# Kernel optimization log

Hardware: AMD Instinct MI355X
Metric: run time of the kernel (lower is better)

The kernel has to match this reference:

```python
import jax, jax.numpy as jnp
import numpy as np

B = 65536
HID = 256
C_K, C_V, C_S, NQ = 4, 8, 4, 4
EMB_OUT = 64  # state_embedding_size - 1


def _spatial_basis():
    # h = w = 5, U = V = 2 -> [5,5,4] Fourier basis
    ph = jnp.arange(1.0, 6.0)[:, None] * jnp.ones((1, 5)) * (np.pi / 5.0)
    pw = jnp.ones((5, 1)) * jnp.arange(1.0, 6.0)[None, :] * (np.pi / 5.0)
    u = jnp.arange(1.0, 3.0)[None, :]
    a = jnp.cos(ph[:, :, None] * u)  # [5,5,2]
    b = jnp.cos(pw[:, :, None] * u)  # [5,5,2]
    return jnp.einsum('hwu,hwv->hwuv', a, b).reshape(5, 5, 4).astype(jnp.float32)


def _conv(x, w, b):
    # x: NHWC, w: HWIO, pad=1, stride=1
    y = jax.lax.conv_general_dilated(x, w, window_strides=(1, 1), padding=[(1, 1), (1, 1)],
                                     dimension_numbers=('NHWC', 'HWIO', 'NHWC'))
    return y + b


def setup_inputs() -> dict:
    key = jax.random.key(0)
    ks = jax.random.split(key, 20)
    s = 0.05
    inp = {
        'X': jax.random.normal(ks[0], (B, 7, 7, 3), jnp.float32),
        'upper_module_hidden_state': jax.random.normal(ks[1], (B, HID), jnp.float32),
        'c1_w': jax.random.normal(ks[2], (5, 5, 3, 8), jnp.float32) * s,
        'c1_b': jax.random.normal(ks[3], (8,), jnp.float32) * s,
        'c2_w': jax.random.normal(ks[4], (3, 3, 8, 12), jnp.float32) * s,
        'c2_b': jax.random.normal(ks[5], (12,), jnp.float32) * s,
    }
    qdims = [(HID, 256), (256, 128), (128, 64), (64, 32), (32, 32)]
    for i, (din, dout) in enumerate(qdims):
        inp[f'qw{i}'] = jax.random.normal(ks[6 + 2 * i], (din, dout), jnp.float32) * s
        inp[f'qb{i}'] = jax.random.normal(ks[7 + 2 * i], (dout,), jnp.float32) * s
    inp['aw0'] = jax.random.normal(ks[16], ((C_V + C_S) * NQ, 32), jnp.float32) * s
    inp['ab0'] = jax.random.normal(ks[17], (32,), jnp.float32) * s
    inp['aw1'] = jax.random.normal(ks[18], (32, EMB_OUT), jnp.float32) * s
    inp['ab1'] = jax.random.normal(ks[19], (EMB_OUT,), jnp.float32) * s
    return inp


def reference(X, upper_module_hidden_state, c1_w, c1_b, c2_w, c2_b,
              qw0, qb0, qw1, qb1, qw2, qb2, qw3, qb3, qw4, qb4,
              aw0, ab0, aw1, ab1):
    b = X.shape[0]
    # vision CNN: [b,7,7,3] -> [b,5,5,8] -> [b,5,5,12]
    O = _conv(_conv(X, c1_w, c1_b), c2_w, c2_b)
    K, V = O[..., :C_K], O[..., C_K:]
    S = jnp.broadcast_to(_spatial_basis(), (b, 5, 5, C_S))
    K = jnp.concatenate([K, S], axis=-1)  # [b,5,5,8]
    V = jnp.concatenate([V, S], axis=-1)  # [b,5,5,12]
    # query MLP -> [b,4,8]
    q = upper_module_hidden_state
    for w, bi in [(qw0, qb0), (qw1, qb1), (qw2, qb2), (qw3, qb3)]:
        q = jax.nn.relu(q @ w + bi)
    q = (q @ qw4 + qb4).reshape(-1, NQ, C_K + C_S)
    # attention logits over 25 spatial positions, softmax over space
    A = jnp.einsum('bhwk,bqk->bhwq', K, q).reshape(b, 25, NQ)
    A = jax.nn.softmax(A, axis=1)
    # apply_alpha: [b,nq,25] @ [b,25,12] -> [b,nq,12]; chunk+cat == reshape
    a = jnp.einsum('bpq,bpd->bqd', A, V.reshape(b, 25, C_V + C_S)).reshape(b, NQ * (C_V + C_S))
    # answer MLP
    return jax.nn.relu(a @ aw0 + ab0) @ aw1 + ab1
```

## Files before the change

### kernel.cpp

```cpp
#include <hip/hip_runtime.h>
#include <hip/hip_bf16.h>

#define NB 65536

typedef __attribute__((ext_vector_type(8))) short short8;
typedef __attribute__((ext_vector_type(4))) short short4v;
typedef __attribute__((ext_vector_type(4))) float f32x4;
typedef __attribute__((ext_vector_type(16))) float f32x16;
typedef __attribute__((ext_vector_type(4))) unsigned int u32x4;

__device__ inline short f2bf(float f) {
    unsigned u = __builtin_bit_cast(unsigned, f);
    unsigned r = (u + 0x7fffu + ((u >> 16) & 1u)) >> 16;
    return (short)(unsigned short)r;
}
__device__ inline float b2f(short s) {
    return __builtin_bit_cast(float, (unsigned)((unsigned short)s) << 16);
}
__device__ inline unsigned pkbf(float lo, float hi) {
    return ((unsigned)(unsigned short)f2bf(hi) << 16) | (unsigned)(unsigned short)f2bf(lo);
}

#define MLPW_CNT 109568
#define WEFF_CNT 51200
#define A0 (MLPW_CNT + WEFF_CNT + 320)
#define A1 (A0 + 2048)
#define A2 (A1 + 2048)
#define A3 (A2 + 100)
#define PREP_TOT (A3 + 512)


__global__ void __launch_bounds__(256) prep_kernel(
    const float* __restrict__ w0, const float* __restrict__ w1,
    const float* __restrict__ w2, const float* __restrict__ w3,
    const float* __restrict__ w4,
    const float* __restrict__ b0, const float* __restrict__ b1,
    const float* __restrict__ b2, const float* __restrict__ b3,
    const float* __restrict__ b4,
    const float* __restrict__ c1w, const float* __restrict__ c1b,
    const float* __restrict__ c2w, const float* __restrict__ c2b,
    const float* __restrict__ aw0, const float* __restrict__ aw1,
    short* __restrict__ wt, short* __restrict__ weff, float* __restrict__ beff,
    short* __restrict__ aw0T, short* __restrict__ aw1T, float* __restrict__ sTab,
    float* __restrict__ biasP)
{
    int idx = blockIdx.x * 256 + threadIdx.x;
    if (idx < MLPW_CNT) {
        const float* W; int N, KT, base;
        if (idx < 65536)       { W = w0; N = 256; KT = 16; base = 0; }
        else if (idx < 98304)  { W = w1; N = 128; KT = 16; base = 65536; }
        else if (idx < 106496) { W = w2; N = 64;  KT = 8;  base = 98304; }
        else if (idx < 108544) { W = w3; N = 32;  KT = 4;  base = 106496; }
        else                   { W = w4; N = 32;  KT = 2;  base = 108544; }
        int i  = idx - base;
        int nt = i / (KT * 512);
        int r1 = i - nt * (KT * 512);
        int kt = r1 >> 9;
        int l  = (r1 & 511) >> 3;
        int j  = i & 7;
        int n  = nt * 32 + (l & 31);
        int k  = kt * 16 + ((l >> 5) << 3) + j;
        wt[idx] = f2bf(W[k * N + n]);
    } else if (idx < MLPW_CNT + WEFF_CNT) {
        int it = idx - MLPW_CNT;
        int n = it / 160, k = it - n * 160;
        float acc = 0.f;
        if (n < 300 && k < 147) {
            int oc = n % 12, p = n / 12, oy = p / 5, ox = p - oy * 5;
            int ci = k % 3,  t = k / 3, iy = t / 7, ix = t - iy * 7;
            for (int y = 0; y < 5; ++y) {
                int ky = iy - y + 1, ly = y - oy + 1;
                if ((unsigned)ky < 5u && (unsigned)ly < 3u) {
                    for (int x = 0; x < 5; ++x) {
                        int kx = ix - x + 1, lx = x - ox + 1;
                        if ((unsigned)kx < 5u && (unsigned)lx < 3u) {
                            const float* p1 = c1w + ((ky * 5 + kx) * 3 + ci) * 8;
                            const float* p2 = c2w + ((ly * 3 + lx) * 8) * 12 + oc;
#pragma unroll
                            for (int c = 0; c < 8; ++c) acc += p1[c] * p2[c * 12];
                        }
                    }
                }
            }
        }
        weff[it] = f2bf(acc);
    } else if (idx < A0) {
        int n = idx - MLPW_CNT - WEFF_CNT;
        float acc = 0.f;
        if (n < 300) {
            int oc = n % 12, p = n / 12, oy = p / 5, ox = p - oy * 5;
            acc = c2b[oc];
            for (int y = 0; y < 5; ++y) {
                int ly = y - oy + 1;
                if ((unsigned)ly < 3u) {
                    for (int x = 0; x < 5; ++x) {
                        int lx = x - ox + 1;
                        if ((unsigned)lx < 3u) {
#pragma unroll
                            for (int c = 0; c < 8; ++c)
                                acc += c2w[((ly * 3 + lx) * 8 + c) * 12 + oc] * c1b[c];
                        }
                    }
                }
            }
        }
        beff[n] = acc;
    } else if (idx < A1) {
        int t = idx - A0;
        int n = t >> 6, k = t & 63;
        aw0T[t] = (k < 48) ? f2bf(aw0[k * 32 + n]) : (short)0;
    } else if (idx < A2) {
        int t = idx - A1;
        int n = t >> 5, k = t & 31;
        aw1T[t] = f2bf(aw1[k * 64 + n]);
    } else if (idx < A3) {
        int i = idx - A2;
        int p = i >> 2, s = i & 3;
        int h = p / 5, w = p - 5 * h;
        int u = (s >> 1) + 1, v = (s & 1) + 1;
        const float PI5 = 0.6283185307179586f;
        sTab[i] = cosf(((float)(h + 1) * PI5) * (float)u) *
                  cosf(((float)(w + 1) * PI5) * (float)v);
    } else if (idx < PREP_TOT) {
        int t = idx - A3;
        const float* B; int N, base;
        if (t < 256)      { B = b0; N = 256; base = 0; }
        else if (t < 384) { B = b1; N = 128; base = 256; }
        else if (t < 448) { B = b2; N = 64;  base = 384; }
        else if (t < 480) { B = b3; N = 32;  base = 448; }
        else              { B = b4; N = 32;  base = 480; }
        int u  = t - base;
        int h  = u / (N / 2);
        int w  = u - h * (N / 2);
        int nt = w >> 4, r = w & 15;
        biasP[t] = B[nt * 32 + (r & 3) + 8 * (r >> 2) + 4 * h];
    }
}

template<int KT>
__device__ inline void stage_load(const short* __restrict__ src,
                                  short8* r, int tid)
{
    constexpr int CNT = (KT * 64 + 255) / 256;
#pragma unroll
    for (int i = 0; i < CNT; ++i) {
        int idx = tid + i * 256;
        if (idx < KT * 64) r[i] = *(const short8*)(src + idx * 8);
    }
}
template<int KT>
__device__ inline void stage_write(short* __restrict__ dst,
                                   const short8* r, int tid)
{
    constexpr int CNT = (KT * 64 + 255) / 256;
#pragma unroll
    for (int i = 0; i < CNT; ++i) {
        int idx = tid + i * 256;
        if (idx < KT * 64) *(short8*)(dst + idx * 8) = r[i];
    }
}

template<int K, int N, bool RELU>
__device__ inline void layerS(const short* __restrict__ wp,
                              const float* __restrict__ bp,
                              const u32x4* __restrict__ inF,
                              u32x4* __restrict__ outF,
                              short* __restrict__ sW0,
                              short* __restrict__ sW1,
                              int tid, int lane, int h)
{
    constexpr int KT = K / 16, NT = N / 32;
    constexpr int CNT = (KT * 64 + 255) / 256;
    short8 tmp[CNT];

    stage_load<KT>(wp, tmp, tid);
    stage_write<KT>(sW0, tmp, tid);
    __syncthreads();

#pragma unroll
    for (int nt = 0; nt < NT; ++nt) {
        short* cur = (nt & 1) ? sW1 : sW0;
        short* nxt = (nt & 1) ? sW0 : sW1;
        if (nt + 1 < NT) stage_load<KT>(wp + (nt + 1) * KT * 512, tmp, tid);

        f32x16 a;
#pragma unroll
        for (int r = 0; r < 16; ++r) a[r] = 0.f;
#pragma unroll
        for (int kt = 0; kt < KT; ++kt) {
            short8 wf = *(const short8*)(cur + kt * 512 + lane * 8);
            a = __builtin_amdgcn_mfma_f32_32x32x16_bf16(
                    wf, __builtin_bit_cast(short8, inF[kt]), a, 0, 0, 0);
        }
        const float* bpp = bp + h * (N / 2) + nt * 16;
        unsigned q[8];
#pragma unroll
        for (int i = 0; i < 8; ++i) {
            float v0 = a[2 * i] + bpp[2 * i];
            float v1 = a[2 * i + 1] + bpp[2 * i + 1];
            if (RELU) { v0 = fmaxf(v0, 0.f); v1 = fmaxf(v1, 0.f); }
            q[i] = pkbf(v0, v1);
        }
        unsigned xq[8];
#pragma unroll
        for (int i = 0; i < 8; ++i) xq[i] = (unsigned)__shfl_xor((int)q[i], 32, 64);
        u32x4 fa, fb;
        if (h == 0) {
            fa[0] = q[0];  fa[1] = q[1];  fa[2] = xq[0]; fa[3] = xq[1];
            fb[0] = q[4];  fb[1] = q[5];  fb[2] = xq[4]; fb[3] = xq[5];
        } else {
            fa[0] = xq[2]; fa[1] = xq[3]; fa[2] = q[2];  fa[3] = q[3];
            fb[0] = xq[6]; fb[1] = xq[7]; fb[2] = q[6];  fb[3] = q[7];
        }
        outF[2 * nt]     = fa;
        outF[2 * nt + 1] = fb;

        if (nt + 1 < NT) stage_write<KT>(nxt, tmp, tid);
        __syncthreads();
    }
}

template<int K>
__device__ inline void layerQ(const short* __restrict__ wp,
                              const float* __restrict__ bp,
                              const u32x4* __restrict__ inF,
                              short* __restrict__ qout,
                              int lane, int h, int r0)
{
    constexpr int KT = K / 16;
    f32x16 a;
#pragma unroll
    for (int r = 0; r < 16; ++r) a[r] = 0.f;
#pragma unroll
    for (int kt = 0; kt < KT; ++kt) {
        short8 wf = *(const short8*)(wp + kt * 512 + lane * 8);
        a = __builtin_amdgcn_mfma_f32_32x32x16_bf16(
                wf, __builtin_bit_cast(short8, inF[kt]), a, 0, 0, 0);
    }
    const float* bpp = bp + h * 16;
    short* qb = qout + (size_t)(r0 + (lane & 31)) * 32 + 4 * h;
    const int fo[8] = {0, 2, 8, 10, 16, 18, 24, 26};
#pragma unroll
    for (int i = 0; i < 8; ++i) {
        float v0 = a[2 * i] + bpp[2 * i];
        float v1 = a[2 * i + 1] + bpp[2 * i + 1];
        *(unsigned*)(qb + fo[i]) = pkbf(v0, v1);
    }
}

__global__ void __launch_bounds__(256, 2) mlp_kernel(
    const float* __restrict__ hid,
    const short* __restrict__ wp,
    const float* __restrict__ biasP,
    short* __restrict__ qout)
{
    __shared__ __align__(16) short sW0[8192];
    __shared__ __align__(16) short sW1[8192];

    const int tid  = threadIdx.x;
    const int lane = tid & 63;
    const int wv   = tid >> 6;
    const int h = lane >> 5, b = lane & 31;
    const int r0 = blockIdx.x * 128 + wv * 32;

    u32x4 A[16], B[16], C[8], D[4], E[2];
    const float* hb = hid + (size_t)(r0 + b) * 256 + h * 8;
#pragma unroll
    for (int kt = 0; kt < 16; ++kt) {
        float4 x = *(const float4*)(hb + kt * 16);
        float4 y = *(const float4*)(hb + kt * 16 + 4);
        u32x4 f;
        f[0] = pkbf(x.x, x.y); f[1] = pkbf(x.z, x.w);
        f[2] = pkbf(y.x, y.y); f[3] = pkbf(y.z, y.w);
        A[kt] = f;
    }
    layerS<256, 256, true>(wp,          biasP,       A, B, sW0, sW1, tid, lane, h);
    layerS<256, 128, true>(wp + 65536,  biasP + 256, B, C, sW0, sW1, tid, lane, h);
    layerS<128,  64, true>(wp + 98304,  biasP + 384, C, D, sW0, sW1, tid, lane, h);
    layerS< 64,  32, true>(wp + 106496, biasP + 448, D, E, sW0, sW1, tid, lane, h);
    layerQ< 32>           (wp + 108544, biasP + 480, E, qout, lane, h, r0);
}

__global__ void __launch_bounds__(256, 4) conv_attn_kernel(
    const float* __restrict__ Xg,
    const short* __restrict__ weffT,
    const float* __restrict__ beff,
    const short* __restrict__ aw0T, const float* __restrict__ ab0,
    const short* __restrict__ aw1T, const float* __restrict__ ab1,
    const float* __restrict__ sTab,
    const short* __restrict__ qb16,
    float* __restrict__ out)
{
    __shared__ __align__(16) short sKV[4][4800];
    __shared__ __align__(16) short sA[4][1024];
    __shared__ __align__(16) short sH[4][512];

    const int tid    = threadIdx.x;
    const int w      = tid >> 6;
    const int lane   = tid & 63;
    const int lanelo = lane & 15;
    const int g      = lane >> 4;
    const int e0     = blockIdx.x * 64 + w * 16;

    short* sX  = &sKV[w][0];
    short* sKc = &sKV[w][0];
    short* sVc = &sKV[w][1600];

#pragma unroll
    for (int i = 0; i < 4; ++i) {
        int t = lane + i * 64;
        if (t < 208) {
            int r = t / 13, c = 147 + (t - r * 13);
            int ch = c >> 3;
            sX[r * 192 + ((ch ^ (r & 7)) << 3) + (c & 7)] = 0;
        }
    }
    {
        const float* xb = Xg + (size_t)e0 * 147;
#define PUTX(IDX, F) { int _i = (IDX); int _r = _i / 147; int _c = _i - _r * 147; \
        int _ch = _c >> 3; sX[_r * 192 + ((_ch ^ (_r & 7)) << 3) + (_c & 7)] = f2bf(F); }
#pragma unroll
        for (int i = 0; i < 10; ++i) {
            int idx4 = lane + i * 64;
            if (idx4 < 588) {
                float4 v = reinterpret_cast<const float4*>(xb)[idx4];
                int base = idx4 * 4;
                PUTX(base + 0, v.x)
                PUTX(base + 1, v.y)
                PUTX(base + 2, v.z)
                PUTX(base + 3, v.w)
            }
        }
#undef PUTX
    }

    short8 af[5];
#pragma unroll
    for (int kt = 0; kt < 5; ++kt) {
        int phys = (kt * 4 + g) ^ (lanelo & 7);
        af[kt] = *(const short8*)(sX + lanelo * 192 + phys * 8);
    }

    short8 bf[3][5];
    {
        const short* wb0 = weffT + lanelo * 160 + g * 8;
        const short* wb1 = weffT + (16 + lanelo) * 160 + g * 8;
#pragma unroll
        for (int kt = 0; kt < 5; ++kt) {
            bf[0][kt] = *(const short8*)(wb0 + kt * 32);
            bf[1][kt] = *(const short8*)(wb1 + kt * 32);
        }
    }
#pragma unroll
    for (int nt = 0; nt < 19; ++nt) {
        if (nt + 2 < 19) {
            const short* wb = weffT + ((nt + 2) * 16 + lanelo) * 160 + g * 8;
#pragma unroll
            for (int kt = 0; kt < 5; ++kt)
                bf[(nt + 2) % 3][kt] = *(const short8*)(wb + kt * 32);
        }
        f32x4 a; a[0] = 0.f; a[1] = 0.f; a[2] = 0.f; a[3] = 0.f;
#pragma unroll
        for (int kt = 0; kt < 5; ++kt)
            a = __builtin_amdgcn_mfma_f32_16x16x32_bf16(af[kt], bf[nt % 3][kt], a, 0, 0, 0);
        int n = nt * 16 + lanelo;
        if (n < 300) {
            float bb = beff[n];
            int p = n / 12, c = n - p * 12;
#pragma unroll
            for (int j = 0; j < 4; ++j) {
                int el = g * 4 + j;
                float v = a[j] + bb;
                if (c < 4) sKc[el * 100 + p * 4 + c]       = f2bf(v);
                else       sVc[el * 200 + p * 8 + (c - 4)] = f2bf(v);
            }
        }
    }

    {
        const int el = lane >> 2, qi = lane & 3;
        short8 qv = *(const short8*)(qb16 + (size_t)(e0 + el) * 32 + qi * 8);
        float qf[8];
#pragma unroll
        for (int i = 0; i < 8; ++i) qf[i] = b2f(qv[i]);

        float lg[25];
        float mx = -1e30f;
#pragma unroll
        for (int p = 0; p < 25; ++p) {
            short4v kv = *(const short4v*)(sKc + el * 100 + p * 4);
            float4 sv = *(const float4*)(sTab + p * 4);
            float s = b2f(kv[0]) * qf[0] + b2f(kv[1]) * qf[1]
                    + b2f(kv[2]) * qf[2] + b2f(kv[3]) * qf[3]
                    + sv.x * qf[4] + sv.y * qf[5]
                    + sv.z * qf[6] + sv.w * qf[7];
            lg[p] = s;
            mx = fmaxf(mx, s);
        }
        float sum = 0.f;
#pragma unroll
        for (int p = 0; p < 25; ++p) { lg[p] = __expf(lg[p] - mx); sum += lg[p]; }
        float inv = 1.f / sum;

        float o[12];
#pragma unroll
        for (int d = 0; d < 12; ++d) o[d] = 0.f;
#pragma unroll
        for (int p = 0; p < 25; ++p) {
            float wgt = lg[p];
            short4v v0 = *(const short4v*)(sVc + el * 200 + p * 8);
            short4v v1 = *(const short4v*)(sVc + el * 200 + p * 8 + 4);
            float4 sv = *(const float4*)(sTab + p * 4);
            o[0] += wgt * b2f(v0[0]); o[1] += wgt * b2f(v0[1]);
            o[2] += wgt * b2f(v0[2]); o[3] += wgt * b2f(v0[3]);
            o[4] += wgt * b2f(v1[0]); o[5] += wgt * b2f(v1[1]);
            o[6] += wgt * b2f(v1[2]); o[7] += wgt * b2f(v1[3]);
            o[8]  += wgt * sv.x; o[9]  += wgt * sv.y;
            o[10] += wgt * sv.z; o[11] += wgt * sv.w;
        }
#pragma unroll
        for (int d = 0; d < 12; ++d) {
            int col = qi * 12 + d;
            int ch = col >> 3;
            sA[w][el * 64 + ((ch ^ (el & 7)) << 3) + (col & 7)] = f2bf(o[d] * inv);
        }
#pragma unroll
        for (int z = 0; z < 4; ++z) {
            int col = 48 + qi * 4 + z;
            int ch = col >> 3;
            sA[w][el * 64 + ((ch ^ (el & 7)) << 3) + (col & 7)] = 0;
        }
    }

    {
        short8 aa0, aa1;
        {
            int p0 = (0 * 4 + g) ^ (lanelo & 7);
            int p1 = (1 * 4 + g) ^ (lanelo & 7);
            aa0 = *(const short8*)(&sA[w][0] + lanelo * 64 + p0 * 8);
            aa1 = *(const short8*)(&sA[w][0] + lanelo * 64 + p1 * 8);
        }
#pragma unroll
        for (int nt2 = 0; nt2 < 2; ++nt2) {
            int n = nt2 * 16 + lanelo;
            short8 bw0 = *(const short8*)(aw0T + n * 64 + g * 8);
            short8 bw1 = *(const short8*)(aw0T + n * 64 + 32 + g * 8);
            f32x4 hh; hh[0] = 0.f; hh[1] = 0.f; hh[2] = 0.f; hh[3] = 0.f;
            hh = __builtin_amdgcn_mfma_f32_16x16x32_bf16(aa0, bw0, hh, 0, 0, 0);
            hh = __builtin_amdgcn_mfma_f32_16x16x32_bf16(aa1, bw1, hh, 0, 0, 0);
            float bb = ab0[n];
#pragma unroll
            for (int j = 0; j < 4; ++j) {
                int row = g * 4 + j;
                int ch = n >> 3;
                float v = fmaxf(hh[j] + bb, 0.f);
                sH[w][row * 32 + ((ch ^ (row & 3)) << 3) + (n & 7)] = f2bf(v);
            }
        }
    }

    {
        short8 ah;
        {
            int ph = (g ^ (lanelo & 3));
            ah = *(const short8*)(&sH[w][0] + lanelo * 32 + ph * 8);
        }
#pragma unroll
        for (int nt3 = 0; nt3 < 4; ++nt3) {
            int n = nt3 * 16 + lanelo;
            short8 bw = *(const short8*)(aw1T + n * 32 + g * 8);
            f32x4 oacc; oacc[0] = 0.f; oacc[1] = 0.f; oacc[2] = 0.f; oacc[3] = 0.f;
            oacc = __builtin_amdgcn_mfma_f32_16x16x32_bf16(ah, bw, oacc, 0, 0, 0);
            float bb = ab1[n];
#pragma unroll
            for (int j = 0; j < 4; ++j) {
                int el = g * 4 + j;
                out[((size_t)e0 + el) * 64 + n] = oacc[j] + bb;
            }
        }
    }
}


extern "C" void kernel_launch(void* const* d_in, const int* in_sizes, int n_in,
                              void* d_out, int out_size, void* d_ws, size_t ws_size,
                              hipStream_t stream)
{
    const float* X   = (const float*)d_in[0];
    const float* hid = (const float*)d_in[1];
    const float* c1w = (const float*)d_in[2];
    const float* c1b = (const float*)d_in[3];
    const float* c2w = (const float*)d_in[4];
    const float* c2b = (const float*)d_in[5];
    const float* qw0 = (const float*)d_in[6];
    const float* qb0 = (const float*)d_in[7];
    const float* qw1 = (const float*)d_in[8];
    const float* qb1 = (const float*)d_in[9];
    const float* qw2 = (const float*)d_in[10];
    const float* qb2 = (const float*)d_in[11];
    const float* qw3 = (const float*)d_in[12];
    const float* qb3 = (const float*)d_in[13];
    const float* qw4 = (const float*)d_in[14];
    const float* qb4 = (const float*)d_in[15];
    const float* aw0 = (const float*)d_in[16];
    const float* ab0 = (const float*)d_in[17];
    const float* aw1 = (const float*)d_in[18];
    const float* ab1 = (const float*)d_in[19];

    float* out   = (float*)d_out;
    short* qb16  = (short*)d_ws;
    short* wsW   = qb16 + (size_t)NB * 32;
    short* weffT = wsW + MLPW_CNT;
    float* beff  = (float*)(weffT + WEFF_CNT);
    short* aw0T  = (short*)(beff + 320);
    short* aw1T  = aw0T + 2048;
    float* sTab  = (float*)(aw1T + 2048);
    float* biasP = sTab + 100;

    hipLaunchKernelGGL(prep_kernel, dim3((PREP_TOT + 255) / 256), dim3(256), 0, stream,
                       qw0, qw1, qw2, qw3, qw4, qb0, qb1, qb2, qb3, qb4,
                       c1w, c1b, c2w, c2b, aw0, aw1,
                       wsW, weffT, beff, aw0T, aw1T, sTab, biasP);
    hipLaunchKernelGGL(mlp_kernel, dim3(NB / 128), dim3(256), 0, stream,
                       hid, wsW, biasP, qb16);
    hipLaunchKernelGGL(conv_attn_kernel, dim3(NB / 64), dim3(256), 0, stream,
                       X, weffT, beff, aw0T, ab0, aw1T, ab1, sTab, qb16, out);
}
```

Measured before the change: 75.74 us.

## Alias attention scratch buffers into conv LDS pool and simplify X staging

Separate per-wave shared buffers for the attention output and the hidden layer now reuse the conv K/V staging region, which cuts shared memory per block. The smaller footprint is meant to let more blocks reside per CU, up to the launch-bounds limit. X staging changes from float4 loads with per-element divides and an XOR swizzle to row-wise coalesced scalar loads into a padded 168-stride layout, which removes the index arithmetic. The cost is possible LDS bank conflicts on the unswizzled fragment reads, and a correctness risk if the aliased regions are still live when they are overwritten.

```diff
diff --git a/kernel.cpp b/kernel.cpp
--- a/kernel.cpp
+++ b/kernel.cpp
@@ -291,9 +291,7 @@
     const short* __restrict__ qb16,
     float* __restrict__ out)
 {
-    __shared__ __align__(16) short sKV[4][4800];
-    __shared__ __align__(16) short sA[4][1024];
-    __shared__ __align__(16) short sH[4][512];
+    __shared__ __align__(16) short sPool[4][4800];
 
     const int tid    = threadIdx.x;
     const int w      = tid >> 6;
@@ -302,44 +300,37 @@
     const int g      = lane >> 4;
     const int e0     = blockIdx.x * 64 + w * 16;
 
-    short* sX  = &sKV[w][0];
-    short* sKc = &sKV[w][0];
-    short* sVc = &sKV[w][1600];
+    short* sX  = &sPool[w][0];
+    short* sKc = &sPool[w][0];
+    short* sVc = &sPool[w][1600];
+    short* sAh = &sPool[w][0];
+    short* sHh = &sPool[w][1024];
 
 #pragma unroll
     for (int i = 0; i < 4; ++i) {
-        int t = lane + i * 64;
-        if (t < 208) {
-            int r = t / 13, c = 147 + (t - r * 13);
-            int ch = c >> 3;
-            sX[r * 192 + ((ch ^ (r & 7)) << 3) + (c & 7)] = 0;
-        }
+        int idx = i * 64 + lane;
+        int r = idx >> 4, c = 144 + (idx & 15);
+        sX[r * 168 + c] = 0;
     }
     {
         const float* xb = Xg + (size_t)e0 * 147;
-#define PUTX(IDX, F) { int _i = (IDX); int _r = _i / 147; int _c = _i - _r * 147; \
-        int _ch = _c >> 3; sX[_r * 192 + ((_ch ^ (_r & 7)) << 3) + (_c & 7)] = f2bf(F); }
-#pragma unroll
-        for (int i = 0; i < 10; ++i) {
-            int idx4 = lane + i * 64;
-            if (idx4 < 588) {
-                float4 v = reinterpret_cast<const float4*>(xb)[idx4];
-                int base = idx4 * 4;
-                PUTX(base + 0, v.x)
-                PUTX(base + 1, v.y)
-                PUTX(base + 2, v.z)
-                PUTX(base + 3, v.w)
+#pragma unroll
+        for (int r = 0; r < 16; ++r) {
+            float v0 = xb[r * 147 + lane];
+            float v1 = xb[r * 147 + 64 + lane];
+            sX[r * 168 + lane]      = f2bf(v0);
+            sX[r * 168 + 64 + lane] = f2bf(v1);
+            if (lane < 19) {
+                float v2 = xb[r * 147 + 128 + lane];
+                sX[r * 168 + 128 + lane] = f2bf(v2);
             }
         }
-#undef PUTX
     }
 
     short8 af[5];
 #pragma unroll
-    for (int kt = 0; kt < 5; ++kt) {
-        int phys = (kt * 4 + g) ^ (lanelo & 7);
-        af[kt] = *(const short8*)(sX + lanelo * 192 + phys * 8);
-    }
+    for (int kt = 0; kt < 5; ++kt)
+        af[kt] = *(const short8*)(sX + lanelo * 168 + kt * 32 + g * 8);
 
     short8 bf[3][5];
     {
@@ -422,13 +413,13 @@
         for (int d = 0; d < 12; ++d) {
             int col = qi * 12 + d;
             int ch = col >> 3;
-            sA[w][el * 64 + ((ch ^ (el & 7)) << 3) + (col & 7)] = f2bf(o[d] * inv);
+            sAh[el * 64 + ((ch ^ (el & 7)) << 3) + (col & 7)] = f2bf(o[d] * inv);
         }
 #pragma unroll
         for (int z = 0; z < 4; ++z) {
             int col = 48 + qi * 4 + z;
             int ch = col >> 3;
-            sA[w][el * 64 + ((ch ^ (el & 7)) << 3) + (col & 7)] = 0;
+            sAh[el * 64 + ((ch ^ (el & 7)) << 3) + (col & 7)] = 0;
         }
     }
 
@@ -437,8 +428,8 @@
         {
             int p0 = (0 * 4 + g) ^ (lanelo & 7);
             int p1 = (1 * 4 + g) ^ (lanelo & 7);
-            aa0 = *(const short8*)(&sA[w][0] + lanelo * 64 + p0 * 8);
-            aa1 = *(const short8*)(&sA[w][0] + lanelo * 64 + p1 * 8);
+            aa0 = *(const short8*)(sAh + lanelo * 64 + p0 * 8);
+            aa1 = *(const short8*)(sAh + lanelo * 64 + p1 * 8);
         }
 #pragma unroll
         for (int nt2 = 0; nt2 < 2; ++nt2) {
@@ -454,7 +445,7 @@
                 int row = g * 4 + j;
                 int ch = n >> 3;
                 float v = fmaxf(hh[j] + bb, 0.f);
-                sH[w][row * 32 + ((ch ^ (row & 3)) << 3) + (n & 7)] = f2bf(v);
+                sHh[row * 32 + ((ch ^ (row & 3)) << 3) + (n & 7)] = f2bf(v);
             }
         }
     }
@@ -463,7 +454,7 @@
         short8 ah;
         {
             int ph = (g ^ (lanelo & 3));
-            ah = *(const short8*)(&sH[w][0] + lanelo * 32 + ph * 8);
+            ah = *(const short8*)(sHh + lanelo * 32 + ph * 8);
         }
 #pragma unroll
         for (int nt3 = 0; nt3 < 4; ++nt3) {
```

After: 80.59 us. 1.06x slower.
